# Performance work log

Hardware: AMD Instinct MI355X
Metric: run time of the kernel (lower is better)

## Reference

```python
import jax, jax.numpy as jnp
import numpy as np

TOPK = 9
NUM_CLASSES = 80
EPS = 1e-9
NUM_ANCHORS_LIST = [25600, 6400, 1600]  # FPN levels, strides 8/16/32 on 1280x1280
STRIDES = [8, 16, 32]
GRID = [160, 80, 40]
B, N_GT = 8, 128


def _make_anchors():
    levels = []
    for stride, g in zip(STRIDES, GRID):
        c = (np.arange(g, dtype=np.float32) + 0.5) * stride
        xx, yy = np.meshgrid(c, c)
        half = stride * 2.5  # anchor size = 5*stride
        a = np.stack([xx - half, yy - half, xx + half, yy + half], -1).reshape(-1, 4)
        levels.append(a)
    return jnp.asarray(np.concatenate(levels, 0), jnp.float32)


def setup_inputs() -> dict:
    key = jax.random.key(0)
    k1, k2, k3 = jax.random.split(key, 3)
    cxy = jax.random.uniform(k1, (B, N_GT, 2), minval=0.0, maxval=1280.0)
    wh = jax.random.uniform(k2, (B, N_GT, 2), minval=16.0, maxval=256.0)
    gt_bboxes = jnp.clip(jnp.concatenate([cxy - wh * 0.5, cxy + wh * 0.5], -1), 0.0, 1280.0)
    gt_labels = jax.random.randint(k3, (B, N_GT, 1), 0, NUM_CLASSES)
    # first 100 GTs valid, rest padding
    pad_gt_mask = jnp.broadcast_to((jnp.arange(N_GT) < 100).astype(jnp.float32)[None, :, None], (B, N_GT, 1))
    return {"anchor_bboxes": _make_anchors(), "gt_labels": gt_labels,
            "gt_bboxes": gt_bboxes, "pad_gt_mask": pad_gt_mask, "bg_index": NUM_CLASSES}


def _atss_assign(anchor_bboxes, gt_labels, gt_bboxes, pad_gt_mask, bg_index):
    Bsz, n = gt_bboxes.shape[:2]
    # 1. IoU between gt [B,n,4] and anchors [L,4] -> [B,n,L]
    lt = jnp.maximum(gt_bboxes[..., None, :2], anchor_bboxes[None, None, :, :2])
    rb = jnp.minimum(gt_bboxes[..., None, 2:], anchor_bboxes[None, None, :, 2:])
    whd = jax.nn.relu(rb - lt)
    inter = whd[..., 0] * whd[..., 1]
    area_g = (gt_bboxes[..., 2] - gt_bboxes[..., 0]) * (gt_bboxes[..., 3] - gt_bboxes[..., 1])
    area_a = (anchor_bboxes[:, 2] - anchor_bboxes[:, 0]) * (anchor_bboxes[:, 3] - anchor_bboxes[:, 1])
    ious = inter / (area_g[..., None] + area_a[None, None, :] - inter + 1e-9)

    # 2. center distance [B,n,L]
    gt_centers = (gt_bboxes[..., :2] + gt_bboxes[..., 2:]) * 0.5          # [B,n,2]
    anchor_centers = (anchor_bboxes[:, :2] + anchor_bboxes[:, 2:]) * 0.5  # [L,2]
    d = gt_centers[:, :, None, :] - anchor_centers[None, None, :, :]
    distances = jnp.sqrt(jnp.sum(d * d, -1))

    # 3. per-pyramid-level topk closest anchors
    pad_bool = pad_gt_mask > 0  # [B,n,1]
    offs = [0] + np.cumsum(NUM_ANCHORS_LIST).tolist()[:-1]
    bi = jnp.arange(Bsz)[:, None, None]
    gi = jnp.arange(n)[None, :, None]
    in_topk_list, idx_list = [], []
    for ll, off in zip(NUM_ANCHORS_LIST, offs):
        dist_l = jax.lax.dynamic_slice_in_dim(distances, off, ll, axis=-1)
        _, idx = jax.lax.top_k(-dist_l, TOPK)  # smallest distances, [B,n,K]
        idx_list.append(idx + off)
        idx_m = jnp.where(pad_bool, idx, 0)
        # scatter-count instead of giant one_hot: [B,n,ll]
        cnt = jnp.zeros((Bsz, n, ll), distances.dtype).at[bi, gi, idx_m].add(1.0)
        in_topk_list.append(jnp.where(cnt > 1, 0.0, cnt))
    is_in_topk = jnp.concatenate(in_topk_list, -1)   # [B,n,L]
    topk_idxs = jnp.concatenate(idx_list, -1)        # [B,n,K*num_levels]

    # 4. iou threshold = mean + std of candidate ious (unbiased std as torch)
    iou_candidates = ious * is_in_topk
    cand = jnp.take_along_axis(iou_candidates, topk_idxs, axis=-1)
    thr = jnp.mean(cand, -1, keepdims=True) + jnp.std(cand, -1, keepdims=True, ddof=1)
    is_in_topk = jnp.where(iou_candidates > thr, is_in_topk, 0.0)

    # 6. anchor centers inside gt boxes
    x = anchor_centers[None, None, :, 0]
    y = anchor_centers[None, None, :, 1]
    l_ = x - gt_bboxes[..., 0:1]
    t_ = y - gt_bboxes[..., 1:2]
    r_ = gt_bboxes[..., 2:3] - x
    b_ = gt_bboxes[..., 3:4] - y
    min_ltrb = jnp.minimum(jnp.minimum(l_, t_), jnp.minimum(r_, b_))
    is_in_gts = (min_ltrb > EPS).astype(gt_bboxes.dtype)

    mask_positive = is_in_topk * is_in_gts * pad_gt_mask  # [B,n,L]
    mask_positive_sum = mask_positive.sum(-2)              # [B,L]

    # 8. anchor assigned to multiple gts -> keep highest-iou gt
    max_idx = jnp.argmax(ious, axis=-2)  # [B,L]
    is_max_iou = (jnp.arange(n)[None, :, None] == max_idx[:, None, :]).astype(ious.dtype)
    mask_multi = mask_positive_sum[:, None, :] > 1
    mask_positive = jnp.where(mask_multi, is_max_iou, mask_positive)
    mask_positive_sum = mask_positive.sum(-2)

    assigned_gt_index = jnp.argmax(mask_positive, axis=-2)  # [B,L]
    assigned_labels = jnp.take_along_axis(gt_labels[..., 0], assigned_gt_index, axis=1)
    assigned_labels = jnp.where(mask_positive_sum > 0, assigned_labels, bg_index)
    assigned_bboxes = jnp.take_along_axis(gt_bboxes, assigned_gt_index[..., None], axis=1)  # [B,L,4]
    one_hot = jax.nn.one_hot(assigned_labels, NUM_CLASSES + 1, dtype=gt_bboxes.dtype)
    keep = jnp.asarray([i for i in range(NUM_CLASSES + 1) if i != bg_index])
    assigned_scores = one_hot[..., keep]  # [B,L,C]
    return assigned_labels, assigned_bboxes, assigned_scores


def reference(anchor_bboxes, gt_labels, gt_bboxes, pad_gt_mask, bg_index):
    return _atss_assign(anchor_bboxes, gt_labels, gt_bboxes, pad_gt_mask, bg_index)
```

## Files before the change

kernel.cpp:

```cpp
#include <hip/hip_runtime.h>
#include <math.h>

#define TOPK   9
#define NCLS   80
#define BATCH  8
#define NGT    128
#define NA     33600
#define OFF1   25600
#define OFF2   32000

__device__ __forceinline__ void anchor_center(int a, float& cx, float& cy) {
    int j, gr, st;
    if (a < OFF1)      { j = a;        gr = 160; st = 8;  }
    else if (a < OFF2) { j = a - OFF1; gr = 80;  st = 16; }
    else               { j = a - OFF2; gr = 40;  st = 32; }
    int row = j / gr;
    int col = j - row * gr;
    cx = (float)(col * st + (st >> 1));
    cy = (float)(row * st + (st >> 1));
}
__device__ __forceinline__ float anchor_half(int a) {
    return (a < OFF1) ? 20.0f : (a < OFF2 ? 40.0f : 80.0f);
}
__device__ __forceinline__ float anchor_area(int a) {
    return (a < OFF1) ? 1600.0f : (a < OFF2 ? 6400.0f : 25600.0f);
}

__device__ __forceinline__ float iou_ga(float gx1, float gy1, float gx2, float gy2,
                                        float ax1, float ay1, float ax2, float ay2,
                                        float area_a) {
    float ltx = fmaxf(gx1, ax1), lty = fmaxf(gy1, ay1);
    float rbx = fminf(gx2, ax2), rby = fminf(gy2, ay2);
    float w = fmaxf(__fsub_rn(rbx, ltx), 0.0f);
    float h = fmaxf(__fsub_rn(rby, lty), 0.0f);
    float inter = __fmul_rn(w, h);
    float ag = __fmul_rn(__fsub_rn(gx2, gx1), __fsub_rn(gy2, gy1));
    float denom = __fadd_rn(__fsub_rn(__fadd_rn(ag, area_a), inter), 1e-9f);
    return inter / denom;
}

__device__ __forceinline__ bool dless(float da, int ia, float db, int ib) {
    return (da < db) || (da == db && ia < ib);
}

__launch_bounds__(128)
__global__ void atss_window_kernel(const float* __restrict__ gt_bboxes,
                                   const float* __restrict__ pad_mask,
                                   int* __restrict__ claim_cnt,
                                   int* __restrict__ claim_gt) {
    const int pair = blockIdx.x;
    const int b = pair >> 7;
    const int g = pair & 127;
    if (pad_mask[b * NGT + g] <= 0.0f) return;

    const int tid = threadIdx.x;
    __shared__ float sd[75];
    __shared__ int   sj[75];
    __shared__ float sx[75], sy[75];
    __shared__ float cand_iou[27];
    __shared__ int   cand_a[27];
    __shared__ int   cand_ok[27];
    __shared__ float thr;

    const float4 gtb = *reinterpret_cast<const float4*>(gt_bboxes + (size_t)(b * NGT + g) * 4);
    const float gcx = __fmul_rn(__fadd_rn(gtb.x, gtb.z), 0.5f);
    const float gcy = __fmul_rn(__fadd_rn(gtb.y, gtb.w), 0.5f);

    const int l  = tid / 25;
    const int c  = tid % 25;
    const int GR = (l == 0) ? 160 : (l == 1 ? 80 : 40);
    const int ST = 8 << l;

    if (tid < 75) {
        const float inv = (l == 0) ? 0.125f : (l == 1 ? 0.0625f : 0.03125f);
        int ix = (int)floorf(__fmul_rn(gcx, inv));
        int iy = (int)floorf(__fmul_rn(gcy, inv));
        ix = min(max(ix, 0), GR - 1);
        iy = min(max(iy, 0), GR - 1);
        const int wx = min(max(ix - 2, 0), GR - 5);
        const int wy = min(max(iy - 2, 0), GR - 5);
        const int col = wx + c % 5;
        const int row = wy + c / 5;
        const float ax = (float)(col * ST + (ST >> 1));
        const float ay = (float)(row * ST + (ST >> 1));
        const float dx = __fsub_rn(gcx, ax);
        const float dy = __fsub_rn(gcy, ay);
        sd[tid] = __fsqrt_rn(__fadd_rn(__fmul_rn(dx, dx), __fmul_rn(dy, dy)));
        sj[tid] = row * GR + col;
        sx[tid] = ax;
        sy[tid] = ay;
    }
    __syncthreads();
    if (tid < 75) {
        const int base = l * 25;
        const float d = sd[tid];
        const int   j = sj[tid];
        int rank = 0;
#pragma unroll
        for (int c2 = 0; c2 < 25; ++c2) {
            rank += dless(sd[base + c2], sj[base + c2], d, j) ? 1 : 0;
        }
        if (rank < TOPK) {
            const int offs = (l == 0) ? 0 : (l == 1 ? OFF1 : OFF2);
            const float hf = (l == 0) ? 20.0f : (l == 1 ? 40.0f : 80.0f);
            const float aa = (l == 0) ? 1600.0f : (l == 1 ? 6400.0f : 25600.0f);
            const float acx = sx[tid], acy = sy[tid];
            const int slot = l * TOPK + rank;
            cand_iou[slot] = iou_ga(gtb.x, gtb.y, gtb.z, gtb.w,
                                    acx - hf, acy - hf, acx + hf, acy + hf, aa);
            cand_a[slot] = j + offs;
            const float l_ = __fsub_rn(acx, gtb.x);
            const float t_ = __fsub_rn(acy, gtb.y);
            const float r_ = __fsub_rn(gtb.z, acx);
            const float b_ = __fsub_rn(gtb.w, acy);
            const float mn = fminf(fminf(l_, t_), fminf(r_, b_));
            cand_ok[slot] = (mn > 1e-9f) ? 1 : 0;
        }
    }
    __syncthreads();
    if (tid == 0) {
        float sum = 0.0f;
#pragma unroll
        for (int k = 0; k < 3 * TOPK; ++k) sum = __fadd_rn(sum, cand_iou[k]);
        const float mean = sum / 27.0f;
        float ss = 0.0f;
#pragma unroll
        for (int k = 0; k < 3 * TOPK; ++k) {
            const float dd = __fsub_rn(cand_iou[k], mean);
            ss = __fadd_rn(ss, __fmul_rn(dd, dd));
        }
        thr = __fadd_rn(mean, __fsqrt_rn(ss / 26.0f));
    }
    __syncthreads();
    if (tid < 3 * TOPK) {
        if (cand_ok[tid] && cand_iou[tid] > thr) {
            const int a = cand_a[tid];
            atomicAdd(&claim_cnt[b * NA + a], 1);
            claim_gt[b * NA + a] = g;
        }
    }
}

__launch_bounds__(256)
__global__ void atss_assign_kernel(const float* __restrict__ gt_bboxes,
                                   const int* __restrict__ gt_labels,
                                   const int* __restrict__ claim_cnt,
                                   const int* __restrict__ claim_gt,
                                   const int* __restrict__ bg_index_p,
                                   float* __restrict__ out_labels,
                                   float* __restrict__ out_bboxes,
                                   float* __restrict__ out_scores) {
    const int t = blockIdx.x * 256 + threadIdx.x;
    const int tid = threadIdx.x;
    const int b = t / NA;
    const int a = t - b * NA;

    const int cnt = claim_cnt[t];
    int  gidx = 0;
    bool pos  = false;
    if (cnt == 1) {
        gidx = claim_gt[t];
        pos = true;
    } else if (cnt > 1) {
        float acx, acy;
        anchor_center(a, acx, acy);
        const float hf = anchor_half(a);
        const float aa = anchor_area(a);
        const float ax1 = acx - hf, ay1 = acy - hf, ax2 = acx + hf, ay2 = acy + hf;
        float best = -1.0f;
        int bestg = 0;
        for (int gg = 0; gg < NGT; ++gg) {
            const float4 gb = *reinterpret_cast<const float4*>(gt_bboxes + (size_t)(b * NGT + gg) * 4);
            const float iou = iou_ga(gb.x, gb.y, gb.z, gb.w, ax1, ay1, ax2, ay2, aa);
            if (iou > best) { best = iou; bestg = gg; }
        }
        gidx = bestg;
        pos = true;
    }

    const float4 bb = *reinterpret_cast<const float4*>(gt_bboxes + (size_t)(b * NGT + gidx) * 4);
    reinterpret_cast<float4*>(out_bboxes)[t] = bb;

    const int lbl = pos ? gt_labels[b * NGT + gidx] : bg_index_p[0];
    out_labels[t] = (float)lbl;

    __shared__ int slbl[256];
    slbl[tid] = pos ? lbl : NCLS;
    __syncthreads();
    const size_t sbase = (size_t)blockIdx.x * 256 * NCLS;
#pragma unroll
    for (int i = 0; i < 20; ++i) {
        const int off  = i * 1024 + tid * 4;
        const int aoff = off / 80;
        const int cls  = off - aoff * 80;
        const int lb   = slbl[aoff];
        float4 v;
        v.x = (cls     == lb) ? 1.0f : 0.0f;
        v.y = (cls + 1 == lb) ? 1.0f : 0.0f;
        v.z = (cls + 2 == lb) ? 1.0f : 0.0f;
        v.w = (cls + 3 == lb) ? 1.0f : 0.0f;
        *reinterpret_cast<float4*>(out_scores + sbase + off) = v;
    }
}

extern "C" void kernel_launch(void* const* d_in, const int* in_sizes, int n_in,
                              void* d_out, int out_size, void* d_ws, size_t ws_size,
                              hipStream_t stream) {
    const float* anchors   = (const float*)d_in[0];
    const int*   gt_labels = (const int*)d_in[1];
    const float* gt_bboxes = (const float*)d_in[2];
    const float* pad_mask  = (const float*)d_in[3];
    const int*   bg_index  = (const int*)d_in[4];
    (void)anchors; (void)in_sizes; (void)n_in; (void)out_size; (void)ws_size;

    float* out        = (float*)d_out;
    float* out_labels = out;
    float* out_bboxes = out + (size_t)BATCH * NA;
    float* out_scores = out + (size_t)BATCH * NA * 5;

    int* claim_cnt = (int*)d_ws;
    int* claim_gt  = claim_cnt + BATCH * NA;

    hipMemsetAsync(claim_cnt, 0, (size_t)BATCH * NA * sizeof(int), stream);

    atss_window_kernel<<<BATCH * NGT, 128, 0, stream>>>(gt_bboxes, pad_mask, claim_cnt, claim_gt);

    atss_assign_kernel<<<(BATCH * NA) / 256, 256, 0, stream>>>(
        gt_bboxes, gt_labels, claim_cnt, claim_gt, bg_index,
        out_labels, out_bboxes, out_scores);
}
```

Before: 138.0 us.

## Split one-hot score writing into separate kernel with nontemporal stores

Moves the one-hot score writing out of the assign kernel into its own wide-grid kernel, which reads per-anchor labels from a workspace array. All output writes now use nontemporal stores. The goal is to spread the dominant ~86MB score write across more threads and to keep streaming output from polluting the cache. In exchange it adds a kernel launch and a round trip of the label array through global memory.

After: 146.9 us. 6.5% more time.

```diff
diff --git a/kernel.cpp b/kernel.cpp
--- a/kernel.cpp
+++ b/kernel.cpp
@@ -8,6 +8,8 @@
 #define NA     33600
 #define OFF1   25600
 #define OFF2   32000
+
+typedef float vfloat4 __attribute__((ext_vector_type(4)));
 
 __device__ __forceinline__ void anchor_center(int a, float& cx, float& cy) {
     int j, gr, st;
@@ -142,16 +144,15 @@
 }
 
 __launch_bounds__(256)
-__global__ void atss_assign_kernel(const float* __restrict__ gt_bboxes,
-                                   const int* __restrict__ gt_labels,
-                                   const int* __restrict__ claim_cnt,
-                                   const int* __restrict__ claim_gt,
-                                   const int* __restrict__ bg_index_p,
-                                   float* __restrict__ out_labels,
-                                   float* __restrict__ out_bboxes,
-                                   float* __restrict__ out_scores) {
+__global__ void atss_resolve_kernel(const float* __restrict__ gt_bboxes,
+                                    const int* __restrict__ gt_labels,
+                                    const int* __restrict__ claim_cnt,
+                                    const int* __restrict__ claim_gt,
+                                    const int* __restrict__ bg_index_p,
+                                    float* __restrict__ out_labels,
+                                    float* __restrict__ out_bboxes,
+                                    int* __restrict__ lbl_arr) {
     const int t = blockIdx.x * 256 + threadIdx.x;
-    const int tid = threadIdx.x;
     const int b = t / NA;
     const int a = t - b * NA;
 
@@ -178,28 +179,31 @@
         pos = true;
     }
 
-    const float4 bb = *reinterpret_cast<const float4*>(gt_bboxes + (size_t)(b * NGT + gidx) * 4);
-    reinterpret_cast<float4*>(out_bboxes)[t] = bb;
+    const vfloat4 bb = *reinterpret_cast<const vfloat4*>(gt_bboxes + (size_t)(b * NGT + gidx) * 4);
+    __builtin_nontemporal_store(bb, reinterpret_cast<vfloat4*>(out_bboxes) + t);
 
     const int lbl = pos ? gt_labels[b * NGT + gidx] : bg_index_p[0];
-    out_labels[t] = (float)lbl;
-
-    __shared__ int slbl[256];
-    slbl[tid] = pos ? lbl : NCLS;
-    __syncthreads();
-    const size_t sbase = (size_t)blockIdx.x * 256 * NCLS;
-#pragma unroll
-    for (int i = 0; i < 20; ++i) {
-        const int off  = i * 1024 + tid * 4;
-        const int aoff = off / 80;
-        const int cls  = off - aoff * 80;
-        const int lb   = slbl[aoff];
-        float4 v;
-        v.x = (cls     == lb) ? 1.0f : 0.0f;
-        v.y = (cls + 1 == lb) ? 1.0f : 0.0f;
-        v.z = (cls + 2 == lb) ? 1.0f : 0.0f;
-        v.w = (cls + 3 == lb) ? 1.0f : 0.0f;
-        *reinterpret_cast<float4*>(out_scores + sbase + off) = v;
+    __builtin_nontemporal_store((float)lbl, out_labels + t);
+
+    lbl_arr[t] = pos ? lbl : NCLS;
+}
+
+__launch_bounds__(256)
+__global__ void atss_scores_kernel(const int* __restrict__ lbl_arr,
+                                   float* __restrict__ out_scores) {
+    const int base = blockIdx.x * 1024 + threadIdx.x;
+#pragma unroll
+    for (int i = 0; i < 4; ++i) {
+        const int q    = base + i * 256;
+        const int aoff = q / 20;
+        const int c4   = (q - aoff * 20) * 4;
+        const int lb   = lbl_arr[aoff];
+        vfloat4 v;
+        v.x = (c4     == lb) ? 1.0f : 0.0f;
+        v.y = (c4 + 1 == lb) ? 1.0f : 0.0f;
+        v.z = (c4 + 2 == lb) ? 1.0f : 0.0f;
+        v.w = (c4 + 3 == lb) ? 1.0f : 0.0f;
+        __builtin_nontemporal_store(v, reinterpret_cast<vfloat4*>(out_scores) + q);
     }
 }
 
@@ -220,12 +224,15 @@
 
     int* claim_cnt = (int*)d_ws;
     int* claim_gt  = claim_cnt + BATCH * NA;
+    int* lbl_arr   = claim_gt + BATCH * NA;
 
     hipMemsetAsync(claim_cnt, 0, (size_t)BATCH * NA * sizeof(int), stream);
 
     atss_window_kernel<<<BATCH * NGT, 128, 0, stream>>>(gt_bboxes, pad_mask, claim_cnt, claim_gt);
 
-    atss_assign_kernel<<<(BATCH * NA) / 256, 256, 0, stream>>>(
+    atss_resolve_kernel<<<(BATCH * NA) / 256, 256, 0, stream>>>(
         gt_bboxes, gt_labels, claim_cnt, claim_gt, bg_index,
-        out_labels, out_bboxes, out_scores);
-}
+        out_labels, out_bboxes, lbl_arr);
+
+    atss_scores_kernel<<<(BATCH * NA * (NCLS / 4)) / 1024, 256, 0, stream>>>(lbl_arr, out_scores);
+}
```

## Fuse memset, window and assign kernels into one cooperative grid-synced kernel

Applied to the files above, without the earlier changes.

Replaces the memset plus two kernel launches with a single cooperative kernel of 1050 blocks. Each block zeroes its slice of the claim counters, then the first 1024 blocks run the per-GT top-k window and claim step, and all blocks do the per-anchor assignment and one-hot write. `grid.sync()` separates the phases. This removes two launch and inter-kernel gaps, but all 1050 blocks must be resident at once, two grid-wide barriers are added, and the launch return code is not checked.

Result: slower. 367.0 us (+165.9%).

```diff
diff --git a/kernel.cpp b/kernel.cpp
--- a/kernel.cpp
+++ b/kernel.cpp
@@ -1,5 +1,8 @@
 #include <hip/hip_runtime.h>
+#include <hip/hip_cooperative_groups.h>
 #include <math.h>
+
+namespace cg = cooperative_groups;
 
 #define TOPK   9
 #define NCLS   80
@@ -43,17 +46,20 @@
     return (da < db) || (da == db && ia < ib);
 }
 
-__launch_bounds__(128)
-__global__ void atss_window_kernel(const float* __restrict__ gt_bboxes,
-                                   const float* __restrict__ pad_mask,
-                                   int* __restrict__ claim_cnt,
-                                   int* __restrict__ claim_gt) {
-    const int pair = blockIdx.x;
-    const int b = pair >> 7;
-    const int g = pair & 127;
-    if (pad_mask[b * NGT + g] <= 0.0f) return;
-
+__launch_bounds__(256)
+__global__ void atss_fused_kernel(const float* __restrict__ gt_bboxes,
+                                  const int* __restrict__ gt_labels,
+                                  const float* __restrict__ pad_mask,
+                                  const int* __restrict__ bg_index_p,
+                                  int* __restrict__ claim_cnt,
+                                  int* __restrict__ claim_gt,
+                                  float* __restrict__ out_labels,
+                                  float* __restrict__ out_bboxes,
+                                  float* __restrict__ out_scores) {
+    cg::grid_group grid = cg::this_grid();
     const int tid = threadIdx.x;
+    const int t   = blockIdx.x * 256 + tid;
+
     __shared__ float sd[75];
     __shared__ int   sj[75];
     __shared__ float sx[75], sy[75];
@@ -61,145 +67,146 @@
     __shared__ int   cand_a[27];
     __shared__ int   cand_ok[27];
     __shared__ float thr;
-
-    const float4 gtb = *reinterpret_cast<const float4*>(gt_bboxes + (size_t)(b * NGT + g) * 4);
-    const float gcx = __fmul_rn(__fadd_rn(gtb.x, gtb.z), 0.5f);
-    const float gcy = __fmul_rn(__fadd_rn(gtb.y, gtb.w), 0.5f);
-
-    const int l  = tid / 25;
-    const int c  = tid % 25;
-    const int GR = (l == 0) ? 160 : (l == 1 ? 80 : 40);
-    const int ST = 8 << l;
-
-    if (tid < 75) {
-        const float inv = (l == 0) ? 0.125f : (l == 1 ? 0.0625f : 0.03125f);
-        int ix = (int)floorf(__fmul_rn(gcx, inv));
-        int iy = (int)floorf(__fmul_rn(gcy, inv));
-        ix = min(max(ix, 0), GR - 1);
-        iy = min(max(iy, 0), GR - 1);
-        const int wx = min(max(ix - 2, 0), GR - 5);
-        const int wy = min(max(iy - 2, 0), GR - 5);
-        const int col = wx + c % 5;
-        const int row = wy + c / 5;
-        const float ax = (float)(col * ST + (ST >> 1));
-        const float ay = (float)(row * ST + (ST >> 1));
-        const float dx = __fsub_rn(gcx, ax);
-        const float dy = __fsub_rn(gcy, ay);
-        sd[tid] = __fsqrt_rn(__fadd_rn(__fmul_rn(dx, dx), __fmul_rn(dy, dy)));
-        sj[tid] = row * GR + col;
-        sx[tid] = ax;
-        sy[tid] = ay;
-    }
-    __syncthreads();
-    if (tid < 75) {
-        const int base = l * 25;
-        const float d = sd[tid];
-        const int   j = sj[tid];
-        int rank = 0;
-#pragma unroll
-        for (int c2 = 0; c2 < 25; ++c2) {
-            rank += dless(sd[base + c2], sj[base + c2], d, j) ? 1 : 0;
-        }
-        if (rank < TOPK) {
-            const int offs = (l == 0) ? 0 : (l == 1 ? OFF1 : OFF2);
-            const float hf = (l == 0) ? 20.0f : (l == 1 ? 40.0f : 80.0f);
-            const float aa = (l == 0) ? 1600.0f : (l == 1 ? 6400.0f : 25600.0f);
-            const float acx = sx[tid], acy = sy[tid];
-            const int slot = l * TOPK + rank;
-            cand_iou[slot] = iou_ga(gtb.x, gtb.y, gtb.z, gtb.w,
-                                    acx - hf, acy - hf, acx + hf, acy + hf, aa);
-            cand_a[slot] = j + offs;
-            const float l_ = __fsub_rn(acx, gtb.x);
-            const float t_ = __fsub_rn(acy, gtb.y);
-            const float r_ = __fsub_rn(gtb.z, acx);
-            const float b_ = __fsub_rn(gtb.w, acy);
-            const float mn = fminf(fminf(l_, t_), fminf(r_, b_));
-            cand_ok[slot] = (mn > 1e-9f) ? 1 : 0;
+    __shared__ int   slbl[256];
+
+    claim_cnt[t] = 0;
+    grid.sync();
+
+    if (blockIdx.x < BATCH * NGT) {
+        const int b = blockIdx.x >> 7;
+        const int g = blockIdx.x & 127;
+        if (pad_mask[b * NGT + g] > 0.0f) {
+            const float4 gtb = *reinterpret_cast<const float4*>(gt_bboxes + (size_t)(b * NGT + g) * 4);
+            const float gcx = __fmul_rn(__fadd_rn(gtb.x, gtb.z), 0.5f);
+            const float gcy = __fmul_rn(__fadd_rn(gtb.y, gtb.w), 0.5f);
+
+            const int l  = tid / 25;
+            const int c  = tid % 25;
+            const int GR = (l == 0) ? 160 : (l == 1 ? 80 : 40);
+            const int ST = 8 << l;
+
+            if (tid < 75) {
+                const float inv = (l == 0) ? 0.125f : (l == 1 ? 0.0625f : 0.03125f);
+                int ix = (int)floorf(__fmul_rn(gcx, inv));
+                int iy = (int)floorf(__fmul_rn(gcy, inv));
+                ix = min(max(ix, 0), GR - 1);
+                iy = min(max(iy, 0), GR - 1);
+                const int wx = min(max(ix - 2, 0), GR - 5);
+                const int wy = min(max(iy - 2, 0), GR - 5);
+                const int col = wx + c % 5;
+                const int row = wy + c / 5;
+                const float ax = (float)(col * ST + (ST >> 1));
+                const float ay = (float)(row * ST + (ST >> 1));
+                const float dx = __fsub_rn(gcx, ax);
+                const float dy = __fsub_rn(gcy, ay);
+                sd[tid] = __fsqrt_rn(__fadd_rn(__fmul_rn(dx, dx), __fmul_rn(dy, dy)));
+                sj[tid] = row * GR + col;
+                sx[tid] = ax;
+                sy[tid] = ay;
+            }
+            __syncthreads();
+            if (tid < 75) {
+                const int base = l * 25;
+                const float d = sd[tid];
+                const int   j = sj[tid];
+                int rank = 0;
+#pragma unroll
+                for (int c2 = 0; c2 < 25; ++c2) {
+                    rank += dless(sd[base + c2], sj[base + c2], d, j) ? 1 : 0;
+                }
+                if (rank < TOPK) {
+                    const int offs = (l == 0) ? 0 : (l == 1 ? OFF1 : OFF2);
+                    const float hf = (l == 0) ? 20.0f : (l == 1 ? 40.0f : 80.0f);
+                    const float aa = (l == 0) ? 1600.0f : (l == 1 ? 6400.0f : 25600.0f);
+                    const float acx = sx[tid], acy = sy[tid];
+                    const int slot = l * TOPK + rank;
+                    cand_iou[slot] = iou_ga(gtb.x, gtb.y, gtb.z, gtb.w,
+                                            acx - hf, acy - hf, acx + hf, acy + hf, aa);
+                    cand_a[slot] = j + offs;
+                    const float l_ = __fsub_rn(acx, gtb.x);
+                    const float t_ = __fsub_rn(acy, gtb.y);
+                    const float r_ = __fsub_rn(gtb.z, acx);
+                    const float b_ = __fsub_rn(gtb.w, acy);
+                    const float mn = fminf(fminf(l_, t_), fminf(r_, b_));
+                    cand_ok[slot] = (mn > 1e-9f) ? 1 : 0;
+                }
+            }
+            __syncthreads();
+            if (tid == 0) {
+                float sum = 0.0f;
+#pragma unroll
+                for (int k = 0; k < 3 * TOPK; ++k) sum = __fadd_rn(sum, cand_iou[k]);
+                const float mean = sum / 27.0f;
+                float ss = 0.0f;
+#pragma unroll
+                for (int k = 0; k < 3 * TOPK; ++k) {
+                    const float dd = __fsub_rn(cand_iou[k], mean);
+                    ss = __fadd_rn(ss, __fmul_rn(dd, dd));
+                }
+                thr = __fadd_rn(mean, __fsqrt_rn(ss / 26.0f));
+            }
+            __syncthreads();
+            if (tid < 3 * TOPK) {
+                if (cand_ok[tid] && cand_iou[tid] > thr) {
+                    const int a = cand_a[tid];
+                    atomicAdd(&claim_cnt[b * NA + a], 1);
+                    claim_gt[b * NA + a] = g;
+                }
+            }
         }
     }
-    __syncthreads();
-    if (tid == 0) {
-        float sum = 0.0f;
-#pragma unroll
-        for (int k = 0; k < 3 * TOPK; ++k) sum = __fadd_rn(sum, cand_iou[k]);
-        const float mean = sum / 27.0f;
-        float ss = 0.0f;
-#pragma unroll
-        for (int k = 0; k < 3 * TOPK; ++k) {
-            const float dd = __fsub_rn(cand_iou[k], mean);
-            ss = __fadd_rn(ss, __fmul_rn(dd, dd));
+    __threadfence();
+    grid.sync();
+
+    {
+        const int b = t / NA;
+        const int a = t - b * NA;
+
+        const int cnt = claim_cnt[t];
+        int  gidx = 0;
+        bool pos  = false;
+        if (cnt == 1) {
+            gidx = claim_gt[t];
+            pos = true;
+        } else if (cnt > 1) {
+            float acx, acy;
+            anchor_center(a, acx, acy);
+            const float hf = anchor_half(a);
+            const float aa = anchor_area(a);
+            const float ax1 = acx - hf, ay1 = acy - hf, ax2 = acx + hf, ay2 = acy + hf;
+            float best = -1.0f;
+            int bestg = 0;
+            for (int gg = 0; gg < NGT; ++gg) {
+                const float4 gb = *reinterpret_cast<const float4*>(gt_bboxes + (size_t)(b * NGT + gg) * 4);
+                const float iou = iou_ga(gb.x, gb.y, gb.z, gb.w, ax1, ay1, ax2, ay2, aa);
+                if (iou > best) { best = iou; bestg = gg; }
+            }
+            gidx = bestg;
+            pos = true;
         }
-        thr = __fadd_rn(mean, __fsqrt_rn(ss / 26.0f));
-    }
-    __syncthreads();
-    if (tid < 3 * TOPK) {
-        if (cand_ok[tid] && cand_iou[tid] > thr) {
-            const int a = cand_a[tid];
-            atomicAdd(&claim_cnt[b * NA + a], 1);
-            claim_gt[b * NA + a] = g;
+
+        const float4 bb = *reinterpret_cast<const float4*>(gt_bboxes + (size_t)(b * NGT + gidx) * 4);
+        reinterpret_cast<float4*>(out_bboxes)[t] = bb;
+
+        const int lbl = pos ? gt_labels[b * NGT + gidx] : bg_index_p[0];
+        out_labels[t] = (float)lbl;
+
+        slbl[tid] = pos ? lbl : NCLS;
+        __syncthreads();
+        const size_t sbase = (size_t)blockIdx.x * 256 * NCLS;
+#pragma unroll
+        for (int i = 0; i < 20; ++i) {
+            const int off  = i * 1024 + tid * 4;
+            const int aoff = off / 80;
+            const int cls  = off - aoff * 80;
+            const int lb   = slbl[aoff];
+            float4 v;
+            v.x = (cls     == lb) ? 1.0f : 0.0f;
+            v.y = (cls + 1 == lb) ? 1.0f : 0.0f;
+            v.z = (cls + 2 == lb) ? 1.0f : 0.0f;
+            v.w = (cls + 3 == lb) ? 1.0f : 0.0f;
+            *reinterpret_cast<float4*>(out_scores + sbase + off) = v;
         }
-    }
-}
-
-__launch_bounds__(256)
-__global__ void atss_assign_kernel(const float* __restrict__ gt_bboxes,
-                                   const int* __restrict__ gt_labels,
-                                   const int* __restrict__ claim_cnt,
-                                   const int* __restrict__ claim_gt,
-                                   const int* __restrict__ bg_index_p,
-                                   float* __restrict__ out_labels,
-                                   float* __restrict__ out_bboxes,
-                                   float* __restrict__ out_scores) {
-    const int t = blockIdx.x * 256 + threadIdx.x;
-    const int tid = threadIdx.x;
-    const int b = t / NA;
-    const int a = t - b * NA;
-
-    const int cnt = claim_cnt[t];
-    int  gidx = 0;
-    bool pos  = false;
-    if (cnt == 1) {
-        gidx = claim_gt[t];
-        pos = true;
-    } else if (cnt > 1) {
-        float acx, acy;
-        anchor_center(a, acx, acy);
-        const float hf = anchor_half(a);
-        const float aa = anchor_area(a);
-        const float ax1 = acx - hf, ay1 = acy - hf, ax2 = acx + hf, ay2 = acy + hf;
-        float best = -1.0f;
-        int bestg = 0;
-        for (int gg = 0; gg < NGT; ++gg) {
-            const float4 gb = *reinterpret_cast<const float4*>(gt_bboxes + (size_t)(b * NGT + gg) * 4);
-            const float iou = iou_ga(gb.x, gb.y, gb.z, gb.w, ax1, ay1, ax2, ay2, aa);
-            if (iou > best) { best = iou; bestg = gg; }
-        }
-        gidx = bestg;
-        pos = true;
-    }
-
-    const float4 bb = *reinterpret_cast<const float4*>(gt_bboxes + (size_t)(b * NGT + gidx) * 4);
-    reinterpret_cast<float4*>(out_bboxes)[t] = bb;
-
-    const int lbl = pos ? gt_labels[b * NGT + gidx] : bg_index_p[0];
-    out_labels[t] = (float)lbl;
-
-    __shared__ int slbl[256];
-    slbl[tid] = pos ? lbl : NCLS;
-    __syncthreads();
-    const size_t sbase = (size_t)blockIdx.x * 256 * NCLS;
-#pragma unroll
-    for (int i = 0; i < 20; ++i) {
-        const int off  = i * 1024 + tid * 4;
-        const int aoff = off / 80;
-        const int cls  = off - aoff * 80;
-        const int lb   = slbl[aoff];
-        float4 v;
-        v.x = (cls     == lb) ? 1.0f : 0.0f;
-        v.y = (cls + 1 == lb) ? 1.0f : 0.0f;
-        v.z = (cls + 2 == lb) ? 1.0f : 0.0f;
-        v.w = (cls + 3 == lb) ? 1.0f : 0.0f;
-        *reinterpret_cast<float4*>(out_scores + sbase + off) = v;
     }
 }
 
@@ -221,11 +228,12 @@
     int* claim_cnt = (int*)d_ws;
     int* claim_gt  = claim_cnt + BATCH * NA;
 
-    hipMemsetAsync(claim_cnt, 0, (size_t)BATCH * NA * sizeof(int), stream);
-
-    atss_window_kernel<<<BATCH * NGT, 128, 0, stream>>>(gt_bboxes, pad_mask, claim_cnt, claim_gt);
-
-    atss_assign_kernel<<<(BATCH * NA) / 256, 256, 0, stream>>>(
-        gt_bboxes, gt_labels, claim_cnt, claim_gt, bg_index,
-        out_labels, out_bboxes, out_scores);
-}
+    void* args[] = {
+        (void*)&gt_bboxes, (void*)&gt_labels, (void*)&pad_mask, (void*)&bg_index,
+        (void*)&claim_cnt, (void*)&claim_gt,
+        (void*)&out_labels, (void*)&out_bboxes, (void*)&out_scores,
+    };
+    hipLaunchCooperativeKernel((void*)atss_fused_kernel,
+                               dim3((BATCH * NA) / 256), dim3(256),
+                               args, 0, stream);
+}
```

## Fuse ATSS window selection and assignment into one per-chunk kernel

Applied to the files above, without the earlier changes.

Replaces the memset, the per-GT window kernel and the per-anchor assign kernel with a single kernel. Each block owns a 320-anchor chunk of one image and recomputes top-9 candidates, IoU thresholds and claims for all 128 GTs in shared memory, keeping only the claims that fall in its chunk. This removes the global atomics, the workspace memset and two extra launches. In exchange, the candidate selection work is duplicated across all 105 chunks per image, and a serial insertion sort runs per thread.

After: 246.4 us. 1.79x slower.

```diff
diff --git a/kernel.cpp b/kernel.cpp
--- a/kernel.cpp
+++ b/kernel.cpp
@@ -8,6 +8,8 @@
 #define NA     33600
 #define OFF1   25600
 #define OFF2   32000
+#define CHUNK  320
+#define NCHUNK 105
 
 __device__ __forceinline__ void anchor_center(int a, float& cx, float& cy) {
     int j, gr, st;
@@ -43,157 +45,178 @@
     return (da < db) || (da == db && ia < ib);
 }
 
-__launch_bounds__(128)
-__global__ void atss_window_kernel(const float* __restrict__ gt_bboxes,
-                                   const float* __restrict__ pad_mask,
-                                   int* __restrict__ claim_cnt,
-                                   int* __restrict__ claim_gt) {
-    const int pair = blockIdx.x;
-    const int b = pair >> 7;
-    const int g = pair & 127;
-    if (pad_mask[b * NGT + g] <= 0.0f) return;
-
-    const int tid = threadIdx.x;
-    __shared__ float sd[75];
-    __shared__ int   sj[75];
-    __shared__ float sx[75], sy[75];
-    __shared__ float cand_iou[27];
-    __shared__ int   cand_a[27];
-    __shared__ int   cand_ok[27];
-    __shared__ float thr;
-
-    const float4 gtb = *reinterpret_cast<const float4*>(gt_bboxes + (size_t)(b * NGT + g) * 4);
-    const float gcx = __fmul_rn(__fadd_rn(gtb.x, gtb.z), 0.5f);
-    const float gcy = __fmul_rn(__fadd_rn(gtb.y, gtb.w), 0.5f);
-
-    const int l  = tid / 25;
-    const int c  = tid % 25;
-    const int GR = (l == 0) ? 160 : (l == 1 ? 80 : 40);
-    const int ST = 8 << l;
-
-    if (tid < 75) {
-        const float inv = (l == 0) ? 0.125f : (l == 1 ? 0.0625f : 0.03125f);
+__launch_bounds__(256, 4)
+__global__ void atss_onepass_kernel(const float* __restrict__ gt_bboxes,
+                                    const int* __restrict__ gt_labels,
+                                    const float* __restrict__ pad_mask,
+                                    const int* __restrict__ bg_index_p,
+                                    float* __restrict__ out_labels,
+                                    float* __restrict__ out_bboxes,
+                                    float* __restrict__ out_scores) {
+    const int tid   = threadIdx.x;
+    const int b     = blockIdx.x / NCHUNK;
+    const int chunk = blockIdx.x - b * NCHUNK;
+    const int abase = chunk * CHUNK;
+
+    __shared__ float4 sBox[NGT];
+    __shared__ int    sLbl[NGT];
+    __shared__ float  sPad[NGT];
+    __shared__ float  cIou[NGT * 27];
+    __shared__ int    cPack[NGT * 27];
+    __shared__ float  sThr[NGT];
+    __shared__ int    sCnt[CHUNK];
+    __shared__ int    sG[CHUNK];
+    __shared__ int    sOutL[CHUNK];
+
+    if (tid < NGT) {
+        sBox[tid] = *reinterpret_cast<const float4*>(gt_bboxes + (size_t)(b * NGT + tid) * 4);
+        sLbl[tid] = gt_labels[b * NGT + tid];
+        sPad[tid] = pad_mask[b * NGT + tid];
+    }
+    for (int s = tid; s < CHUNK; s += 256) sCnt[s] = 0;
+    __syncthreads();
+
+    for (int u = tid; u < 3 * NGT; u += 256) {
+        const int l = u >> 7;
+        const int g = u & (NGT - 1);
+        if (sPad[g] <= 0.0f) continue;
+
+        const int   GR   = (l == 0) ? 160 : (l == 1 ? 80 : 40);
+        const int   ST   = 8 << l;
+        const float inv  = (l == 0) ? 0.125f : (l == 1 ? 0.0625f : 0.03125f);
+        const int   offs = (l == 0) ? 0 : (l == 1 ? OFF1 : OFF2);
+        const float hf   = (l == 0) ? 20.0f : (l == 1 ? 40.0f : 80.0f);
+        const float aa   = (l == 0) ? 1600.0f : (l == 1 ? 6400.0f : 25600.0f);
+
+        const float4 gb  = sBox[g];
+        const float  gcx = __fmul_rn(__fadd_rn(gb.x, gb.z), 0.5f);
+        const float  gcy = __fmul_rn(__fadd_rn(gb.y, gb.w), 0.5f);
+
         int ix = (int)floorf(__fmul_rn(gcx, inv));
         int iy = (int)floorf(__fmul_rn(gcy, inv));
         ix = min(max(ix, 0), GR - 1);
         iy = min(max(iy, 0), GR - 1);
         const int wx = min(max(ix - 2, 0), GR - 5);
         const int wy = min(max(iy - 2, 0), GR - 5);
-        const int col = wx + c % 5;
-        const int row = wy + c / 5;
-        const float ax = (float)(col * ST + (ST >> 1));
-        const float ay = (float)(row * ST + (ST >> 1));
-        const float dx = __fsub_rn(gcx, ax);
-        const float dy = __fsub_rn(gcy, ay);
-        sd[tid] = __fsqrt_rn(__fadd_rn(__fmul_rn(dx, dx), __fmul_rn(dy, dy)));
-        sj[tid] = row * GR + col;
-        sx[tid] = ax;
-        sy[tid] = ay;
-    }
-    __syncthreads();
-    if (tid < 75) {
-        const int base = l * 25;
-        const float d = sd[tid];
-        const int   j = sj[tid];
-        int rank = 0;
-#pragma unroll
-        for (int c2 = 0; c2 < 25; ++c2) {
-            rank += dless(sd[base + c2], sj[base + c2], d, j) ? 1 : 0;
-        }
-        if (rank < TOPK) {
-            const int offs = (l == 0) ? 0 : (l == 1 ? OFF1 : OFF2);
-            const float hf = (l == 0) ? 20.0f : (l == 1 ? 40.0f : 80.0f);
-            const float aa = (l == 0) ? 1600.0f : (l == 1 ? 6400.0f : 25600.0f);
-            const float acx = sx[tid], acy = sy[tid];
-            const int slot = l * TOPK + rank;
-            cand_iou[slot] = iou_ga(gtb.x, gtb.y, gtb.z, gtb.w,
-                                    acx - hf, acy - hf, acx + hf, acy + hf, aa);
-            cand_a[slot] = j + offs;
-            const float l_ = __fsub_rn(acx, gtb.x);
-            const float t_ = __fsub_rn(acy, gtb.y);
-            const float r_ = __fsub_rn(gtb.z, acx);
-            const float b_ = __fsub_rn(gtb.w, acy);
+
+        float bd[TOPK]; int bj[TOPK]; float bx[TOPK]; float by[TOPK];
+#pragma unroll
+        for (int k = 0; k < TOPK; ++k) { bd[k] = INFINITY; bj[k] = 0x7FFFFFFF; bx[k] = 0.f; by[k] = 0.f; }
+        for (int r = 0; r < 5; ++r) {
+            for (int c = 0; c < 5; ++c) {
+                const int col = wx + c, row = wy + r;
+                const float ax = (float)(col * ST + (ST >> 1));
+                const float ay = (float)(row * ST + (ST >> 1));
+                const float dx = __fsub_rn(gcx, ax);
+                const float dy = __fsub_rn(gcy, ay);
+                const float d  = __fsqrt_rn(__fadd_rn(__fmul_rn(dx, dx), __fmul_rn(dy, dy)));
+                const int   j  = row * GR + col;
+                if (dless(d, j, bd[TOPK - 1], bj[TOPK - 1])) {
+                    bd[TOPK - 1] = d; bj[TOPK - 1] = j; bx[TOPK - 1] = ax; by[TOPK - 1] = ay;
+#pragma unroll
+                    for (int k = TOPK - 1; k > 0; --k) {
+                        if (dless(bd[k], bj[k], bd[k - 1], bj[k - 1])) {
+                            float t0 = bd[k]; bd[k] = bd[k - 1]; bd[k - 1] = t0;
+                            int   t1 = bj[k]; bj[k] = bj[k - 1]; bj[k - 1] = t1;
+                            float t2 = bx[k]; bx[k] = bx[k - 1]; bx[k - 1] = t2;
+                            float t3 = by[k]; by[k] = by[k - 1]; by[k - 1] = t3;
+                        }
+                    }
+                }
+            }
+        }
+#pragma unroll
+        for (int k = 0; k < TOPK; ++k) {
+            const float acx = bx[k], acy = by[k];
+            const float iou = iou_ga(gb.x, gb.y, gb.z, gb.w,
+                                     acx - hf, acy - hf, acx + hf, acy + hf, aa);
+            const float l_ = __fsub_rn(acx, gb.x);
+            const float t_ = __fsub_rn(acy, gb.y);
+            const float r_ = __fsub_rn(gb.z, acx);
+            const float b_ = __fsub_rn(gb.w, acy);
             const float mn = fminf(fminf(l_, t_), fminf(r_, b_));
-            cand_ok[slot] = (mn > 1e-9f) ? 1 : 0;
-        }
-    }
-    __syncthreads();
-    if (tid == 0) {
+            const int   ok = (mn > 1e-9f) ? 1 : 0;
+            const int   slot = g * 27 + l * TOPK + k;
+            cIou[slot]  = iou;
+            cPack[slot] = (bj[k] + offs) | (ok << 20);
+        }
+    }
+    __syncthreads();
+
+    if (tid < NGT && sPad[tid] > 0.0f) {
+        const float* cv = &cIou[tid * 27];
         float sum = 0.0f;
 #pragma unroll
-        for (int k = 0; k < 3 * TOPK; ++k) sum = __fadd_rn(sum, cand_iou[k]);
+        for (int k = 0; k < 27; ++k) sum = __fadd_rn(sum, cv[k]);
         const float mean = sum / 27.0f;
         float ss = 0.0f;
 #pragma unroll
-        for (int k = 0; k < 3 * TOPK; ++k) {
-            const float dd = __fsub_rn(cand_iou[k], mean);
+        for (int k = 0; k < 27; ++k) {
+            const float dd = __fsub_rn(cv[k], mean);
             ss = __fadd_rn(ss, __fmul_rn(dd, dd));
         }
-        thr = __fadd_rn(mean, __fsqrt_rn(ss / 26.0f));
-    }
-    __syncthreads();
-    if (tid < 3 * TOPK) {
-        if (cand_ok[tid] && cand_iou[tid] > thr) {
-            const int a = cand_a[tid];
-            atomicAdd(&claim_cnt[b * NA + a], 1);
-            claim_gt[b * NA + a] = g;
-        }
-    }
-}
-
-__launch_bounds__(256)
-__global__ void atss_assign_kernel(const float* __restrict__ gt_bboxes,
-                                   const int* __restrict__ gt_labels,
-                                   const int* __restrict__ claim_cnt,
-                                   const int* __restrict__ claim_gt,
-                                   const int* __restrict__ bg_index_p,
-                                   float* __restrict__ out_labels,
-                                   float* __restrict__ out_bboxes,
-                                   float* __restrict__ out_scores) {
-    const int t = blockIdx.x * 256 + threadIdx.x;
-    const int tid = threadIdx.x;
-    const int b = t / NA;
-    const int a = t - b * NA;
-
-    const int cnt = claim_cnt[t];
-    int  gidx = 0;
-    bool pos  = false;
-    if (cnt == 1) {
-        gidx = claim_gt[t];
-        pos = true;
-    } else if (cnt > 1) {
-        float acx, acy;
-        anchor_center(a, acx, acy);
-        const float hf = anchor_half(a);
-        const float aa = anchor_area(a);
-        const float ax1 = acx - hf, ay1 = acy - hf, ax2 = acx + hf, ay2 = acy + hf;
-        float best = -1.0f;
-        int bestg = 0;
-        for (int gg = 0; gg < NGT; ++gg) {
-            const float4 gb = *reinterpret_cast<const float4*>(gt_bboxes + (size_t)(b * NGT + gg) * 4);
-            const float iou = iou_ga(gb.x, gb.y, gb.z, gb.w, ax1, ay1, ax2, ay2, aa);
-            if (iou > best) { best = iou; bestg = gg; }
-        }
-        gidx = bestg;
-        pos = true;
-    }
-
-    const float4 bb = *reinterpret_cast<const float4*>(gt_bboxes + (size_t)(b * NGT + gidx) * 4);
-    reinterpret_cast<float4*>(out_bboxes)[t] = bb;
-
-    const int lbl = pos ? gt_labels[b * NGT + gidx] : bg_index_p[0];
-    out_labels[t] = (float)lbl;
-
-    __shared__ int slbl[256];
-    slbl[tid] = pos ? lbl : NCLS;
-    __syncthreads();
-    const size_t sbase = (size_t)blockIdx.x * 256 * NCLS;
-#pragma unroll
-    for (int i = 0; i < 20; ++i) {
+        sThr[tid] = __fadd_rn(mean, __fsqrt_rn(ss / 26.0f));
+    }
+    __syncthreads();
+
+    for (int e = tid; e < NGT * 27; e += 256) {
+        const int g = e / 27;
+        if (sPad[g] <= 0.0f) continue;
+        const int pk = cPack[e];
+        if ((pk >> 20) & 1) {
+            if (cIou[e] > sThr[g]) {
+                const int a = pk & 0xFFFFF;
+                const int s = a - abase;
+                if (s >= 0 && s < CHUNK) {
+                    atomicAdd(&sCnt[s], 1);
+                    sG[s] = g;
+                }
+            }
+        }
+    }
+    __syncthreads();
+
+    const int bg = bg_index_p[0];
+    for (int s = tid; s < CHUNK; s += 256) {
+        const int a   = abase + s;
+        const int cnt = sCnt[s];
+        int  gidx = 0;
+        bool pos  = false;
+        if (cnt == 1) {
+            gidx = sG[s];
+            pos = true;
+        } else if (cnt > 1) {
+            float acx, acy;
+            anchor_center(a, acx, acy);
+            const float hf2 = anchor_half(a);
+            const float aa2 = anchor_area(a);
+            const float ax1 = acx - hf2, ay1 = acy - hf2, ax2 = acx + hf2, ay2 = acy + hf2;
+            float best = -1.0f;
+            int bestg = 0;
+            for (int gg = 0; gg < NGT; ++gg) {
+                const float4 gbb = sBox[gg];
+                const float iou = iou_ga(gbb.x, gbb.y, gbb.z, gbb.w, ax1, ay1, ax2, ay2, aa2);
+                if (iou > best) { best = iou; bestg = gg; }
+            }
+            gidx = bestg;
+            pos = true;
+        }
+
+        const int t = b * NA + a;
+        reinterpret_cast<float4*>(out_bboxes)[t] = sBox[gidx];
+        const int lbl = pos ? sLbl[gidx] : bg;
+        out_labels[t] = (float)lbl;
+        sOutL[s] = pos ? lbl : NCLS;
+    }
+    __syncthreads();
+
+    const size_t sbase = (size_t)(b * NA + abase) * NCLS;
+#pragma unroll
+    for (int i = 0; i < 25; ++i) {
         const int off  = i * 1024 + tid * 4;
         const int aoff = off / 80;
         const int cls  = off - aoff * 80;
-        const int lb   = slbl[aoff];
+        const int lb   = sOutL[aoff];
         float4 v;
         v.x = (cls     == lb) ? 1.0f : 0.0f;
         v.y = (cls + 1 == lb) ? 1.0f : 0.0f;
@@ -211,21 +234,14 @@
     const float* gt_bboxes = (const float*)d_in[2];
     const float* pad_mask  = (const float*)d_in[3];
     const int*   bg_index  = (const int*)d_in[4];
-    (void)anchors; (void)in_sizes; (void)n_in; (void)out_size; (void)ws_size;
+    (void)anchors; (void)in_sizes; (void)n_in; (void)out_size; (void)d_ws; (void)ws_size;
 
     float* out        = (float*)d_out;
     float* out_labels = out;
     float* out_bboxes = out + (size_t)BATCH * NA;
     float* out_scores = out + (size_t)BATCH * NA * 5;
 
-    int* claim_cnt = (int*)d_ws;
-    int* claim_gt  = claim_cnt + BATCH * NA;
-
-    hipMemsetAsync(claim_cnt, 0, (size_t)BATCH * NA * sizeof(int), stream);
-
-    atss_window_kernel<<<BATCH * NGT, 128, 0, stream>>>(gt_bboxes, pad_mask, claim_cnt, claim_gt);
-
-    atss_assign_kernel<<<(BATCH * NA) / 256, 256, 0, stream>>>(
-        gt_bboxes, gt_labels, claim_cnt, claim_gt, bg_index,
+    atss_onepass_kernel<<<BATCH * NCHUNK, 256, 0, stream>>>(
+        gt_bboxes, gt_labels, pad_mask, bg_index,
         out_labels, out_bboxes, out_scores);
 }
```
